# Kernel optimization log

Hardware: AMD Instinct MI355X
Metric: run time of the kernel (lower is better)

The kernel has to match this reference:

```python
import jax, jax.numpy as jnp
import numpy as np

N, C, HW, HEADS = 2048, 16, 8, 4
F = C * HW * HW  # 1024
E = 16384
EPS = 1e-5
NEG_SLOPE = 0.2


def _bn(x, g, b):
    # training-mode BatchNorm2d over (N, H, W)
    m = x.mean(axis=(0, 2, 3), keepdims=True)
    v = x.var(axis=(0, 2, 3), keepdims=True)
    return (x - m) * jax.lax.rsqrt(v + EPS) * g[None, :, None, None] + b[None, :, None, None]


def _conv1x1(x, w, b):
    # 1x1 conv == per-pixel linear: w is [out_c, in_c]
    return jnp.einsum('nchw,oc->nohw', x, w) + b[None, :, None, None]


def _gatv2(xf, edge_index, wl, bl, wr, br, att, bias_gat):
    # xf: [N, F] node features
    xl = (xf @ wl + bl).reshape(N, HEADS, F)  # source-side transform (lin_l)
    xr = (xf @ wr + br).reshape(N, HEADS, F)  # target-side transform (lin_r)
    src, dst = edge_index[0], edge_index[1]
    loops = jnp.arange(N)
    # PyG default: remove existing self loops (mask them) then add self loops
    src_f = jnp.concatenate([src, loops])
    dst_f = jnp.concatenate([dst, loops])
    valid = jnp.concatenate([src != dst, jnp.ones((N,), bool)])
    xj = xl[src_f]                                   # [E+N, HEADS, F] gather
    e = jax.nn.leaky_relu(xj + xr[dst_f], negative_slope=NEG_SLOPE)
    logits = jnp.einsum('ehf,hf->eh', e, att)        # [E+N, HEADS]
    logits = jnp.where(valid[:, None], logits, -jnp.inf)
    mx = jax.lax.stop_gradient(jax.ops.segment_max(logits, dst_f, num_segments=N))
    expv = jnp.where(valid[:, None], jnp.exp(logits - mx[dst_f]), 0.0)
    denom = jax.ops.segment_sum(expv, dst_f, num_segments=N)
    alpha = expv / denom[dst_f]                      # segment softmax over incoming edges
    out = jax.ops.segment_sum(alpha[:, :, None] * xj, dst_f, num_segments=N)  # [N, HEADS, F]
    return out.reshape(N, HEADS * F) + bias_gat


def setup_inputs() -> dict:
    key = jax.random.key(0)
    ks = jax.random.split(key, 8)
    s = 0.02
    return {
        'x': jax.random.normal(ks[0], (N, C, HW, HW), jnp.float32),
        'edge_index': jax.random.randint(ks[1], (2, E), 0, N),
        'w1': jax.random.normal(ks[2], (C, C), jnp.float32) * s,
        'b1': jnp.zeros((C,), jnp.float32),
        'g1': jnp.ones((C,), jnp.float32),
        'be1': jnp.zeros((C,), jnp.float32),
        'wl': jax.random.normal(ks[3], (F, HEADS * F), jnp.float32) * s,
        'bl': jnp.zeros((HEADS * F,), jnp.float32),
        'wr': jax.random.normal(ks[4], (F, HEADS * F), jnp.float32) * s,
        'br': jnp.zeros((HEADS * F,), jnp.float32),
        'att': jax.random.normal(ks[5], (HEADS, F), jnp.float32) * s,
        'bias_gat': jnp.zeros((HEADS * F,), jnp.float32),
        'w2': jax.random.normal(ks[6], (C, HEADS * C), jnp.float32) * s,
        'b2': jnp.zeros((C,), jnp.float32),
        'g2': jnp.ones((C,), jnp.float32),
        'be2': jnp.zeros((C,), jnp.float32),
    }


def reference(x, edge_index, w1, b1, g1, be1, wl, bl, wr, br, att, bias_gat, w2, b2, g2, be2):
    res = x
    y = _bn(_conv1x1(x, w1, b1), g1, be1)            # fc1: Conv2d 1x1 + BN
    yf = y.reshape(N, F)
    g = _gatv2(yf, edge_index, wl, bl, wr, br, att, bias_gat)
    g = g.reshape(N, HEADS * C, HW, HW)
    out = _bn(_conv1x1(g, w2, b2), g2, be2)          # fc2: Conv2d 1x1 + BN
    return out + res                                  # DropPath(0.0) == Identity
```

## Files before the change

### kernel.cpp

```cpp
#include <hip/hip_runtime.h>
#include <stdint.h>

#define N_NODES 2048
#define F_DIM   1024
#define HEADS   4
#define NF      4096
#define ROW     8192
#define E_EDGES 16384
#define MAXE    (E_EDGES + N_NODES)
#define BN_EPS  1e-5f
#define NSLOPE  0.2f

typedef unsigned short ushort_t;
typedef __attribute__((ext_vector_type(8))) short bf16x8;
typedef __attribute__((ext_vector_type(4))) float f32x4;
typedef __attribute__((ext_vector_type(8))) unsigned short us8;

__device__ __forceinline__ float b2f(unsigned short u) {
    union { unsigned int i; float f; } x; x.i = ((unsigned int)u) << 16; return x.f;
}
__device__ __forceinline__ unsigned short f2b(float f) {
    union { float f; unsigned int i; } x; x.f = f;
    unsigned int r = x.i + 0x7fffu + ((x.i >> 16) & 1u);
    return (unsigned short)(r >> 16);
}
__device__ __forceinline__ ushort_t ld_canon(const void* src, size_t i, int f32) {
    return f32 ? f2b(((const float*)src)[i]) : ((const ushort_t*)src)[i];
}
__device__ __forceinline__ float ld_f(const void* src, size_t i, int f32) {
    return f32 ? ((const float*)src)[i] : b2f(((const ushort_t*)src)[i]);
}

__device__ __forceinline__ int sniff_i64(const int* ei_raw, int* lds_flag) {
    int t = threadIdx.x;
    if (t < 64) {
        int nz = (ei_raw[2 * t + 1] != 0) ? 1 : 0;
        unsigned long long m = __ballot(nz);
        if (t == 0) *lds_flag = (m == 0ull) ? 1 : 0;
    }
    __syncthreads();
    return *lds_flag;
}

__global__ __launch_bounds__(256) void k_count(
    const int* __restrict__ ei_raw, const ushort_t* __restrict__ x_probe,
    int* __restrict__ counts, int* __restrict__ flags)
{
    __shared__ int sflag;
    int i64 = sniff_i64(ei_raw, &sflag);
    int t = threadIdx.x;
    if (blockIdx.x == 0 && t >= 64 && t < 96) {
        unsigned e = (x_probe[2 * (t - 64)] >> 7) & 0xFF;
        unsigned long long m = __ballot(e >= 0x90u);
        if (t == 64) flags[0] = (__popcll(m) >= 3) ? 1 : 0;
    }
    int idx = blockIdx.x * 256 + t;
    if (idx < E_EDGES) {
        int s = i64 ? ei_raw[2 * idx] : ei_raw[idx];
        int d = i64 ? ei_raw[2 * (E_EDGES + idx)] : ei_raw[E_EDGES + idx];
        if (s != d) atomicAdd(&counts[d], 1);
    } else if (idx < MAXE) {
        atomicAdd(&counts[idx - E_EDGES], 1);
    }
}

__global__ __launch_bounds__(256) void k_scan(
    const int* __restrict__ counts, int* __restrict__ offs, int* __restrict__ cursor)
{
    __shared__ int ts[256];
    int t = threadIdx.x;
    int loc[8]; int tot = 0;
    #pragma unroll
    for (int j = 0; j < 8; ++j) { loc[j] = counts[t * 8 + j]; tot += loc[j]; }
    ts[t] = tot; __syncthreads();
    for (int s = 1; s < 256; s <<= 1) {
        int v = (t >= s) ? ts[t - s] : 0;
        __syncthreads();
        ts[t] += v;
        __syncthreads();
    }
    int run = ts[t] - tot;
    #pragma unroll
    for (int j = 0; j < 8; ++j) {
        offs[t * 8 + j] = run; cursor[t * 8 + j] = run; run += loc[j];
    }
    if (t == 255) offs[2048] = run;
}

__global__ __launch_bounds__(256) void k_scatter(
    const int* __restrict__ ei_raw, int* __restrict__ cursor, int* __restrict__ esrc)
{
    __shared__ int sflag;
    int i64 = sniff_i64(ei_raw, &sflag);
    int idx = blockIdx.x * 256 + threadIdx.x;
    if (idx < E_EDGES) {
        int s = i64 ? ei_raw[2 * idx] : ei_raw[idx];
        int d = i64 ? ei_raw[2 * (E_EDGES + idx)] : ei_raw[E_EDGES + idx];
        if (s != d) esrc[atomicAdd(&cursor[d], 1)] = s;
    } else if (idx < MAXE) {
        int n = idx - E_EDGES;
        esrc[atomicAdd(&cursor[n], 1)] = n;
    }
}

__global__ __launch_bounds__(256) void k_fc1(
    const void* __restrict__ x, const void* __restrict__ w1, const void* __restrict__ b1,
    const int* __restrict__ flags,
    float* __restrict__ y0, float* __restrict__ ps, float* __restrict__ pq)
{
    __shared__ float xs[1024];
    __shared__ float sw[256];
    __shared__ float sb[16];
    int f32 = flags[0];
    int tid = threadIdx.x;
    sw[tid] = ld_f(w1, tid, f32);
    if (tid < 16) sb[tid] = ld_f(b1, tid, f32);
    int wave = tid >> 6, lane = tid & 63;
    float s[4] = {0,0,0,0}, q[4] = {0,0,0,0};
    for (int nn = 0; nn < 8; ++nn) {
        int n = blockIdx.x * 8 + nn;
        __syncthreads();
        #pragma unroll
        for (int i = 0; i < 4; ++i) {
            int idx = tid + i * 256;
            xs[idx] = ld_f(x, (size_t)n * 1024 + idx, f32);
        }
        __syncthreads();
        #pragma unroll
        for (int i = 0; i < 4; ++i) {
            int o = wave * 4 + i;
            float acc = sb[o];
            #pragma unroll
            for (int c = 0; c < 16; ++c) acc += xs[c * 64 + lane] * sw[o * 16 + c];
            y0[(size_t)n * 1024 + o * 64 + lane] = acc;
            s[i] += acc; q[i] += acc * acc;
        }
    }
    #pragma unroll
    for (int i = 0; i < 4; ++i)
        for (int mm = 1; mm < 64; mm <<= 1) {
            s[i] += __shfl_xor(s[i], mm);
            q[i] += __shfl_xor(q[i], mm);
        }
    if (lane == 0)
        #pragma unroll
        for (int i = 0; i < 4; ++i) {
            ps[blockIdx.x * 16 + wave * 4 + i] = s[i];
            pq[blockIdx.x * 16 + wave * 4 + i] = q[i];
        }
}

__global__ __launch_bounds__(256) void k_norm(
    const float* __restrict__ y0, const float* __restrict__ ps, const float* __restrict__ pq,
    const void* __restrict__ g1, const void* __restrict__ be1, const int* __restrict__ flags,
    ushort_t* __restrict__ xf)
{
    __shared__ float red[2][64];
    __shared__ float scs[16], shs[16];
    int f32 = flags[0];
    int t = threadIdx.x, lane = t & 63, wv = t >> 6;
    float s = 0.f, q = 0.f;
    #pragma unroll
    for (int i = 0; i < 16; ++i) { s += ps[i * 256 + t]; q += pq[i * 256 + t]; }
    s += __shfl_xor(s, 16); q += __shfl_xor(q, 16);
    s += __shfl_xor(s, 32); q += __shfl_xor(q, 32);
    if (lane < 16) { red[0][wv * 16 + lane] = s; red[1][wv * 16 + lane] = q; }
    __syncthreads();
    if (t < 16) {
        float S = red[0][t] + red[0][16 + t] + red[0][32 + t] + red[0][48 + t];
        float Q = red[1][t] + red[1][16 + t] + red[1][32 + t] + red[1][48 + t];
        const float inv = 1.0f / 131072.0f;
        float mean = S * inv;
        float var  = Q * inv - mean * mean;
        float sc = ld_f(g1, t, f32) * rsqrtf(var + BN_EPS);
        scs[t] = sc;
        shs[t] = ld_f(be1, t, f32) - mean * sc;
    }
    __syncthreads();
    int base = blockIdx.x * 4096;
    #pragma unroll
    for (int i = 0; i < 16; ++i) {
        int k = base + t + i * 256;
        int ch = (k >> 6) & 15;
        xf[k] = f2b(y0[k] * scs[ch] + shs[ch]);
    }
}

__global__ __launch_bounds__(256) void k_convT(
    const void* __restrict__ wl, const void* __restrict__ wr,
    const int* __restrict__ flags, ushort_t* __restrict__ wT)
{
    __shared__ ushort_t tl[64][65];
    int f32 = flags[0];
    const void* in = blockIdx.z ? wr : wl;
    ushort_t* outT = wT + (size_t)blockIdx.z * 4194304ull;
    int bx = blockIdx.x * 64, by = blockIdx.y * 64;
    #pragma unroll
    for (int i = 0; i < 16; ++i) {
        int idx = threadIdx.x + i * 256;
        int r = idx >> 6, c = idx & 63;
        tl[r][c] = ld_canon(in, (size_t)(by + r) * 4096 + bx + c, f32);
    }
    __syncthreads();
    #pragma unroll
    for (int i = 0; i < 16; ++i) {
        int idx = threadIdx.x + i * 256;
        int r = idx >> 6, c = idx & 63;
        outT[(size_t)(bx + r) * 1024 + by + c] = tl[c][r];
    }
}

__global__ __launch_bounds__(256) void k_gemm(
    const ushort_t* __restrict__ A, const ushort_t* __restrict__ BT,
    const void* __restrict__ blr, const void* __restrict__ brr,
    const int* __restrict__ flags, ushort_t* __restrict__ out)
{
    __shared__ __align__(16) ushort_t smem[16384];
    ushort_t* As0 = smem;
    ushort_t* As1 = smem + 4096;
    ushort_t* Bs0 = smem + 8192;
    ushort_t* Bs1 = smem + 12288;
    ushort_t* cs  = smem;
    int f32 = flags[0];
    int tid = threadIdx.x;
    int wv = tid >> 6, ln = tid & 63;
    int m0 = blockIdx.y * 128, n0 = blockIdx.x * 128;
    int wm = (wv >> 1) * 64, wn = (wv & 1) * 64;
    int lr = ln & 15, quad = ln >> 4;

    f32x4 acc[4][4];
    #pragma unroll
    for (int i = 0; i < 4; ++i)
        #pragma unroll
        for (int j = 0; j < 4; ++j) acc[i][j] = (f32x4){0.f, 0.f, 0.f, 0.f};

    for (int k0 = 0; k0 < 1024; k0 += 64) {
        #pragma unroll
        for (int i = 0; i < 2; ++i) {
            int cbase = i * 256 + wv * 64;
            int ci = cbase + ln;
            int m = ci >> 2, kc = ci & 3;
            const ushort_t* ga = A + (size_t)(m0 + m) * 1024 + k0 + kc * 8;
            __builtin_amdgcn_global_load_lds(
                (const __attribute__((address_space(1))) void*)ga,
                (__attribute__((address_space(3))) void*)(&As0[cbase * 8]), 16, 0, 0);
            __builtin_amdgcn_global_load_lds(
                (const __attribute__((address_space(1))) void*)(ga + 32),
                (__attribute__((address_space(3))) void*)(&As1[cbase * 8]), 16, 0, 0);
            const ushort_t* gb = BT + (size_t)(n0 + m) * 1024 + k0 + kc * 8;
            __builtin_amdgcn_global_load_lds(
                (const __attribute__((address_space(1))) void*)gb,
                (__attribute__((address_space(3))) void*)(&Bs0[cbase * 8]), 16, 0, 0);
            __builtin_amdgcn_global_load_lds(
                (const __attribute__((address_space(1))) void*)(gb + 32),
                (__attribute__((address_space(3))) void*)(&Bs1[cbase * 8]), 16, 0, 0);
        }
        __syncthreads();
        #pragma unroll
        for (int p = 0; p < 2; ++p) {
            const ushort_t* Ap = p ? As1 : As0;
            const ushort_t* Bp = p ? Bs1 : Bs0;
            bf16x8 af[4], bfr[4];
            #pragma unroll
            for (int i = 0; i < 4; ++i)
                af[i] = *(const bf16x8*)(&Ap[(wm + i * 16 + lr) * 32 + quad * 8]);
            #pragma unroll
            for (int j = 0; j < 4; ++j)
                bfr[j] = *(const bf16x8*)(&Bp[(wn + j * 16 + lr) * 32 + quad * 8]);
            #pragma unroll
            for (int i = 0; i < 4; ++i)
                #pragma unroll
                for (int j = 0; j < 4; ++j)
                    acc[i][j] = __builtin_amdgcn_mfma_f32_16x16x32_bf16(af[i], bfr[j], acc[i][j], 0, 0, 0);
        }
        __syncthreads();
    }
    float bj[4];
    #pragma unroll
    for (int j = 0; j < 4; ++j) {
        int colg = n0 + wn + j * 16 + lr;
        bj[j] = (colg < 4096) ? ld_f(blr, colg, f32) : ld_f(brr, colg - 4096, f32);
    }
    #pragma unroll
    for (int ph = 0; ph < 2; ++ph) {
        if ((wv >> 1) == ph) {
            #pragma unroll
            for (int i = 0; i < 4; ++i)
                #pragma unroll
                for (int j = 0; j < 4; ++j) {
                    int col = wn + j * 16 + lr;
                    #pragma unroll
                    for (int r = 0; r < 4; ++r)
                        cs[(i * 16 + quad * 4 + r) * 136 + col] = f2b(acc[i][j][r] + bj[j]);
                }
        }
        __syncthreads();
        #pragma unroll
        for (int rr = 0; rr < 4; ++rr) {
            int slot = rr * 256 + tid;
            int row = slot >> 4, seg = slot & 15;
            us8 v = *(const us8*)&cs[row * 136 + seg * 8];
            *(us8*)(out + (size_t)(m0 + ph * 64 + row) * ROW + n0 + seg * 8) = v;
        }
        __syncthreads();
    }
}

__global__ __launch_bounds__(256) void k_gat(
    const ushort_t* __restrict__ xlr,
    const void* __restrict__ att, const void* __restrict__ bg,
    const int* __restrict__ flags,
    const int* __restrict__ offsets, const int* __restrict__ esrc,
    ushort_t* __restrict__ g)
{
    int pair = blockIdx.x * 4 + (threadIdx.x >> 6);
    int d = pair >> 2, h = pair & 3;
    int l = threadIdx.x & 63;
    int f32 = flags[0];
    int off = offsets[d], deg = offsets[d + 1] - off;
    size_t hF = (size_t)h * F_DIM + l * 16;

    float xrv[16], attv[16];
    {
        const ushort_t* xp = xlr + ((size_t)d * ROW + NF + hF);
        us8 x0 = *(const us8*)xp, x1 = *(const us8*)(xp + 8);
        #pragma unroll
        for (int j = 0; j < 8; ++j) {
            xrv[j] = b2f(x0[j]); xrv[8 + j] = b2f(x1[j]);
            attv[j]     = ld_f(att, hF + j, f32);
            attv[8 + j] = ld_f(att, hF + 8 + j, f32);
        }
    }
    float acc[16];
    #pragma unroll
    for (int j = 0; j < 16; ++j) acc[j] = 0.f;
    float s_run = 0.f;

    for (int c0 = 0; c0 < deg; c0 += 64) {
        int cnt = min(64, deg - c0);
        int eidx = esrc[off + c0 + (l < cnt ? l : 0)];
        int e = 0;
        for (; e + 3 < cnt; e += 4) {
            int i0 = __shfl(eidx, e),     i1 = __shfl(eidx, e + 1);
            int i2 = __shfl(eidx, e + 2), i3 = __shfl(eidx, e + 3);
            const ushort_t* p0 = xlr + ((size_t)i0 * ROW + hF);
            const ushort_t* p1 = xlr + ((size_t)i1 * ROW + hF);
            const ushort_t* p2 = xlr + ((size_t)i2 * ROW + hF);
            const ushort_t* p3 = xlr + ((size_t)i3 * ROW + hF);
            us8 v0[4], v1[4];
            v0[0] = *(const us8*)p0; v1[0] = *(const us8*)(p0 + 8);
            v0[1] = *(const us8*)p1; v1[1] = *(const us8*)(p1 + 8);
            v0[2] = *(const us8*)p2; v1[2] = *(const us8*)(p2 + 8);
            v0[3] = *(const us8*)p3; v1[3] = *(const us8*)(p3 + 8);
            float tt[4];
            #pragma unroll
            for (int k = 0; k < 4; ++k) {
                float t0 = 0.f;
                #pragma unroll
                for (int j = 0; j < 8; ++j) {
                    float u;
                    u = b2f(v0[k][j]) + xrv[j];     u = u > 0.f ? u : NSLOPE * u; t0 += u * attv[j];
                    u = b2f(v1[k][j]) + xrv[8 + j]; u = u > 0.f ? u : NSLOPE * u; t0 += u * attv[8 + j];
                }
                tt[k] = t0;
            }
            #pragma unroll
            for (int mm = 1; mm < 64; mm <<= 1) {
                tt[0] += __shfl_xor(tt[0], mm);
                tt[1] += __shfl_xor(tt[1], mm);
                tt[2] += __shfl_xor(tt[2], mm);
                tt[3] += __shfl_xor(tt[3], mm);
            }
            float w0 = __expf(tt[0]), w1 = __expf(tt[1]);
            float w2v = __expf(tt[2]), w3 = __expf(tt[3]);
            s_run += w0 + w1 + w2v + w3;
            #pragma unroll
            for (int j = 0; j < 8; ++j) {
                acc[j]     += w0 * b2f(v0[0][j]) + w1 * b2f(v0[1][j])
                            + w2v * b2f(v0[2][j]) + w3 * b2f(v0[3][j]);
                acc[8 + j] += w0 * b2f(v1[0][j]) + w1 * b2f(v1[1][j])
                            + w2v * b2f(v1[2][j]) + w3 * b2f(v1[3][j]);
            }
        }
        for (; e < cnt; ++e) {
            int i0 = __shfl(eidx, e);
            const ushort_t* p = xlr + ((size_t)i0 * ROW + hF);
            us8 a0 = *(const us8*)p, a1 = *(const us8*)(p + 8);
            float t0 = 0.f;
            #pragma unroll
            for (int j = 0; j < 8; ++j) {
                float u;
                u = b2f(a0[j]) + xrv[j];     u = u > 0.f ? u : NSLOPE * u; t0 += u * attv[j];
                u = b2f(a1[j]) + xrv[8 + j]; u = u > 0.f ? u : NSLOPE * u; t0 += u * attv[8 + j];
            }
            #pragma unroll
            for (int mm = 1; mm < 64; mm <<= 1) t0 += __shfl_xor(t0, mm);
            float w0 = __expf(t0);
            s_run += w0;
            #pragma unroll
            for (int j = 0; j < 8; ++j) {
                acc[j]     += w0 * b2f(a0[j]);
                acc[8 + j] += w0 * b2f(a1[j]);
            }
        }
    }
    float inv = 1.0f / s_run;
    ushort_t* gp = g + ((size_t)d * NF + hF);
    us8 outv0, outv1;
    #pragma unroll
    for (int j = 0; j < 8; ++j) {
        outv0[j] = f2b(acc[j] * inv + ld_f(bg, hF + j, f32));
        outv1[j] = f2b(acc[8 + j] * inv + ld_f(bg, hF + 8 + j, f32));
    }
    *(us8*)gp = outv0;
    *(us8*)(gp + 8) = outv1;
}

__global__ __launch_bounds__(256) void k_fc2(
    const ushort_t* __restrict__ g, const void* __restrict__ w2, const void* __restrict__ b2,
    const int* __restrict__ flags,
    float* __restrict__ z, float* __restrict__ ps, float* __restrict__ pq)
{
    __shared__ float gs[4096];
    __shared__ float sw[1024];
    __shared__ float sb[16];
    int f32 = flags[0];
    int tid = threadIdx.x;
    #pragma unroll
    for (int i = 0; i < 4; ++i) sw[tid + i * 256] = ld_f(w2, tid + i * 256, f32);
    if (tid < 16) sb[tid] = ld_f(b2, tid, f32);
    int wave = tid >> 6, lane = tid & 63;
    float s[4] = {0,0,0,0}, q[4] = {0,0,0,0};
    for (int nn = 0; nn < 8; ++nn) {
        int n = blockIdx.x * 8 + nn;
        __syncthreads();
        {
            const ushort_t* gp = g + (size_t)n * 4096 + tid * 16;
            us8 v0 = *(const us8*)gp, v1 = *(const us8*)(gp + 8);
            #pragma unroll
            for (int j = 0; j < 8; ++j) {
                gs[tid * 16 + j] = b2f(v0[j]);
                gs[tid * 16 + 8 + j] = b2f(v1[j]);
            }
        }
        __syncthreads();
        #pragma unroll
        for (int i = 0; i < 4; ++i) {
            int o = wave * 4 + i;
            float acc = sb[o];
            #pragma unroll
            for (int k = 0; k < 64; ++k) acc += gs[k * 64 + lane] * sw[o * 64 + k];
            z[(size_t)n * 1024 + o * 64 + lane] = acc;
            s[i] += acc; q[i] += acc * acc;
        }
    }
    #pragma unroll
    for (int i = 0; i < 4; ++i)
        for (int mm = 1; mm < 64; mm <<= 1) {
            s[i] += __shfl_xor(s[i], mm);
            q[i] += __shfl_xor(q[i], mm);
        }
    if (lane == 0)
        #pragma unroll
        for (int i = 0; i < 4; ++i) {
            ps[blockIdx.x * 16 + wave * 4 + i] = s[i];
            pq[blockIdx.x * 16 + wave * 4 + i] = q[i];
        }
}

__global__ __launch_bounds__(256) void k_out(
    const float* __restrict__ z, const void* __restrict__ x,
    const float* __restrict__ ps, const float* __restrict__ pq,
    const void* __restrict__ g2, const void* __restrict__ be2,
    const int* __restrict__ flags, void* __restrict__ out)
{
    __shared__ float red[2][64];
    __shared__ float scs[16], shs[16];
    int f32 = flags[0];
    int t = threadIdx.x, lane = t & 63, wv = t >> 6;
    float s = 0.f, q = 0.f;
    #pragma unroll
    for (int i = 0; i < 16; ++i) { s += ps[i * 256 + t]; q += pq[i * 256 + t]; }
    s += __shfl_xor(s, 16); q += __shfl_xor(q, 16);
    s += __shfl_xor(s, 32); q += __shfl_xor(q, 32);
    if (lane < 16) { red[0][wv * 16 + lane] = s; red[1][wv * 16 + lane] = q; }
    __syncthreads();
    if (t < 16) {
        float S = red[0][t] + red[0][16 + t] + red[0][32 + t] + red[0][48 + t];
        float Q = red[1][t] + red[1][16 + t] + red[1][32 + t] + red[1][48 + t];
        const float inv = 1.0f / 131072.0f;
        float mean = S * inv;
        float var  = Q * inv - mean * mean;
        float sc = ld_f(g2, t, f32) * rsqrtf(var + BN_EPS);
        scs[t] = sc;
        shs[t] = ld_f(be2, t, f32) - mean * sc;
    }
    __syncthreads();
    size_t base = (size_t)blockIdx.x * 8192;
    #pragma unroll
    for (int i = 0; i < 32; ++i) {
        size_t k = base + t + i * 256;
        int ch = ((int)k >> 6) & 15;
        float val = z[k] * scs[ch] + shs[ch] + ld_f(x, k, f32);
        if (f32) ((float*)out)[k] = val;
        else     ((ushort_t*)out)[k] = f2b(val);
    }
}

extern "C" void kernel_launch(void* const* d_in, const int* in_sizes, int n_in,
                              void* d_out, int out_size, void* d_ws, size_t ws_size,
                              hipStream_t stream)
{
    const void* x   = d_in[0];
    const void* ei  = d_in[1];
    const void* w1  = d_in[2];
    const void* b1  = d_in[3];
    const void* g1  = d_in[4];
    const void* be1 = d_in[5];
    const void* wl  = d_in[6];
    const void* bl  = d_in[7];
    const void* wr  = d_in[8];
    const void* br  = d_in[9];
    const void* att = d_in[10];
    const void* bg  = d_in[11];
    const void* w2  = d_in[12];
    const void* b2  = d_in[13];
    const void* g2  = d_in[14];
    const void* be2 = d_in[15];
    (void)in_sizes; (void)n_in; (void)out_size; (void)ws_size;

    char* wsb = (char*)d_ws;
    size_t o = 0;
    auto alloc = [&](size_t bytes) -> void* {
        void* p = wsb + o;
        o = (o + bytes + 255) & ~(size_t)255;
        return p;
    };
    int*      flags = (int*)alloc(256);
    float*    y0    = (float*)alloc(2097152ull * 4);
    float*    z     = y0;
    ushort_t* xf    = (ushort_t*)alloc(2097152ull * 2);
    ushort_t* wT    = (ushort_t*)alloc(8388608ull * 2);
    ushort_t* gbuf  = wT;
    ushort_t* xlr   = (ushort_t*)alloc(16777216ull * 2);
    float* p1s = (float*)alloc(256 * 16 * 4);
    float* p1q = (float*)alloc(256 * 16 * 4);
    float* p2s = (float*)alloc(256 * 16 * 4);
    float* p2q = (float*)alloc(256 * 16 * 4);
    int* counts = (int*)alloc(2048 * 4);
    int* offs   = (int*)alloc(2049 * 4);
    int* cursor = (int*)alloc(2048 * 4);
    int* esrc   = (int*)alloc(MAXE * 4);

    hipMemsetAsync(counts, 0, 2048 * 4, stream);
    k_count<<<72, 256, 0, stream>>>((const int*)ei, (const ushort_t*)x, counts, flags);
    k_scan<<<1, 256, 0, stream>>>(counts, offs, cursor);
    k_scatter<<<72, 256, 0, stream>>>((const int*)ei, cursor, esrc);
    k_fc1<<<256, 256, 0, stream>>>(x, w1, b1, flags, y0, p1s, p1q);
    k_norm<<<512, 256, 0, stream>>>(y0, p1s, p1q, g1, be1, flags, xf);
    k_convT<<<dim3(64, 16, 2), 256, 0, stream>>>(wl, wr, flags, wT);
    k_gemm<<<dim3(64, 16), 256, 0, stream>>>(xf, wT, bl, br, flags, xlr);
    k_gat<<<N_NODES, 256, 0, stream>>>(xlr, att, bg, flags, offs, esrc, gbuf);
    k_fc2<<<256, 256, 0, stream>>>(gbuf, w2, b2, flags, z, p2s, p2q);
    k_out<<<256, 256, 0, stream>>>(z, x, p2s, p2q, g2, be2, flags, d_out);
}
```

Before: 290.7 us.

## Fold BN1 into GEMM weights, merge scan into scatter, prefetch GAT gathers

Several changes at once. The scan is merged into the scatter kernel: every block recomputes the prefix sum of the counts in shared memory, which removes one launch. The BN1 scale is folded into the transposed GAT weights, and its shift goes into a per-column bias correction computed from column sums, so the standalone normalize pass over y0 goes away and fc1 writes bf16 directly. The GAT kernel now runs one 64-thread block per (node, head) and double-buffers its gathered rows to overlap loads with compute. The risks are extra rounding from folding the scale into bf16 weights and a 16-term bias correction recomputed in every GEMM block.

```diff
diff --git a/kernel.cpp b/kernel.cpp
--- a/kernel.cpp
+++ b/kernel.cpp
@@ -64,10 +64,14 @@
     }
 }
 
-__global__ __launch_bounds__(256) void k_scan(
-    const int* __restrict__ counts, int* __restrict__ offs, int* __restrict__ cursor)
-{
+__global__ __launch_bounds__(256) void k_scatter(
+    const int* __restrict__ ei_raw, const int* __restrict__ counts,
+    int* __restrict__ cursor, int* __restrict__ offs, int* __restrict__ esrc)
+{
+    __shared__ int sflag;
+    __shared__ int offl[2048];
     __shared__ int ts[256];
+    int i64 = sniff_i64(ei_raw, &sflag);
     int t = threadIdx.x;
     int loc[8]; int tot = 0;
     #pragma unroll
@@ -81,32 +85,28 @@
     }
     int run = ts[t] - tot;
     #pragma unroll
-    for (int j = 0; j < 8; ++j) {
-        offs[t * 8 + j] = run; cursor[t * 8 + j] = run; run += loc[j];
-    }
-    if (t == 255) offs[2048] = run;
-}
-
-__global__ __launch_bounds__(256) void k_scatter(
-    const int* __restrict__ ei_raw, int* __restrict__ cursor, int* __restrict__ esrc)
-{
-    __shared__ int sflag;
-    int i64 = sniff_i64(ei_raw, &sflag);
-    int idx = blockIdx.x * 256 + threadIdx.x;
+    for (int j = 0; j < 8; ++j) { offl[t * 8 + j] = run; run += loc[j]; }
+    __syncthreads();
+    if (blockIdx.x == 0) {
+        #pragma unroll
+        for (int j = 0; j < 8; ++j) offs[t * 8 + j] = offl[t * 8 + j];
+        if (t == 255) offs[2048] = run;
+    }
+    int idx = blockIdx.x * 256 + t;
     if (idx < E_EDGES) {
         int s = i64 ? ei_raw[2 * idx] : ei_raw[idx];
         int d = i64 ? ei_raw[2 * (E_EDGES + idx)] : ei_raw[E_EDGES + idx];
-        if (s != d) esrc[atomicAdd(&cursor[d], 1)] = s;
+        if (s != d) esrc[offl[d] + atomicAdd(&cursor[d], 1)] = s;
     } else if (idx < MAXE) {
         int n = idx - E_EDGES;
-        esrc[atomicAdd(&cursor[n], 1)] = n;
+        esrc[offl[n] + atomicAdd(&cursor[n], 1)] = n;
     }
 }
 
 __global__ __launch_bounds__(256) void k_fc1(
     const void* __restrict__ x, const void* __restrict__ w1, const void* __restrict__ b1,
     const int* __restrict__ flags,
-    float* __restrict__ y0, float* __restrict__ ps, float* __restrict__ pq)
+    ushort_t* __restrict__ y0b, float* __restrict__ ps, float* __restrict__ pq)
 {
     __shared__ float xs[1024];
     __shared__ float sw[256];
@@ -132,7 +132,7 @@
             float acc = sb[o];
             #pragma unroll
             for (int c = 0; c < 16; ++c) acc += xs[c * 64 + lane] * sw[o * 16 + c];
-            y0[(size_t)n * 1024 + o * 64 + lane] = acc;
+            y0b[(size_t)n * 1024 + o * 64 + lane] = f2b(acc);
             s[i] += acc; q[i] += acc * acc;
         }
     }
@@ -150,51 +150,48 @@
         }
 }
 
-__global__ __launch_bounds__(256) void k_norm(
-    const float* __restrict__ y0, const float* __restrict__ ps, const float* __restrict__ pq,
-    const void* __restrict__ g1, const void* __restrict__ be1, const int* __restrict__ flags,
-    ushort_t* __restrict__ xf)
-{
-    __shared__ float red[2][64];
-    __shared__ float scs[16], shs[16];
-    int f32 = flags[0];
-    int t = threadIdx.x, lane = t & 63, wv = t >> 6;
+__global__ __launch_bounds__(256) void k_bnf1(
+    const float* __restrict__ ps, const float* __restrict__ pq,
+    const void* __restrict__ g1, const void* __restrict__ be1,
+    const int* __restrict__ flags, float* __restrict__ ss)
+{
+    __shared__ float rs[16][16], rq[16][16];
+    int f32 = flags[0];
+    int t = threadIdx.x;
+    int ch = t & 15, seg = t >> 4;
     float s = 0.f, q = 0.f;
-    #pragma unroll
-    for (int i = 0; i < 16; ++i) { s += ps[i * 256 + t]; q += pq[i * 256 + t]; }
-    s += __shfl_xor(s, 16); q += __shfl_xor(q, 16);
-    s += __shfl_xor(s, 32); q += __shfl_xor(q, 32);
-    if (lane < 16) { red[0][wv * 16 + lane] = s; red[1][wv * 16 + lane] = q; }
+    for (int j = 0; j < 16; ++j) {
+        int b = seg * 16 + j;
+        s += ps[b * 16 + ch]; q += pq[b * 16 + ch];
+    }
+    rs[seg][ch] = s; rq[seg][ch] = q;
     __syncthreads();
     if (t < 16) {
-        float S = red[0][t] + red[0][16 + t] + red[0][32 + t] + red[0][48 + t];
-        float Q = red[1][t] + red[1][16 + t] + red[1][32 + t] + red[1][48 + t];
+        float S = 0.f, Q = 0.f;
+        #pragma unroll
+        for (int g = 0; g < 16; ++g) { S += rs[g][t]; Q += rq[g][t]; }
         const float inv = 1.0f / 131072.0f;
         float mean = S * inv;
         float var  = Q * inv - mean * mean;
         float sc = ld_f(g1, t, f32) * rsqrtf(var + BN_EPS);
-        scs[t] = sc;
-        shs[t] = ld_f(be1, t, f32) - mean * sc;
-    }
-    __syncthreads();
-    int base = blockIdx.x * 4096;
-    #pragma unroll
-    for (int i = 0; i < 16; ++i) {
-        int k = base + t + i * 256;
-        int ch = (k >> 6) & 15;
-        xf[k] = f2b(y0[k] * scs[ch] + shs[ch]);
+        ss[t] = sc;
+        ss[16 + t] = ld_f(be1, t, f32) - mean * sc;
     }
 }
 
 __global__ __launch_bounds__(256) void k_convT(
     const void* __restrict__ wl, const void* __restrict__ wr,
-    const int* __restrict__ flags, ushort_t* __restrict__ wT)
+    const int* __restrict__ flags, const float* __restrict__ ss,
+    ushort_t* __restrict__ wT, float* __restrict__ csum)
 {
     __shared__ ushort_t tl[64][65];
+    __shared__ float red[4][64];
     int f32 = flags[0];
     const void* in = blockIdx.z ? wr : wl;
     ushort_t* outT = wT + (size_t)blockIdx.z * 4194304ull;
     int bx = blockIdx.x * 64, by = blockIdx.y * 64;
+    int ch = by >> 6;
+    float sc = ss[ch];
     #pragma unroll
     for (int i = 0; i < 16; ++i) {
         int idx = threadIdx.x + i * 256;
@@ -206,13 +203,23 @@
     for (int i = 0; i < 16; ++i) {
         int idx = threadIdx.x + i * 256;
         int r = idx >> 6, c = idx & 63;
-        outT[(size_t)(bx + r) * 1024 + by + c] = tl[c][r];
-    }
+        outT[(size_t)(bx + r) * 1024 + by + c] = f2b(b2f(tl[c][r]) * sc);
+    }
+    int c = threadIdx.x & 63, quarter = threadIdx.x >> 6;
+    float p = 0.f;
+    #pragma unroll
+    for (int rr = 0; rr < 16; ++rr) p += b2f(tl[quarter * 16 + rr][c]);
+    red[quarter][c] = p;
+    __syncthreads();
+    if (quarter == 0)
+        csum[(size_t)ch * 8192 + blockIdx.z * 4096 + bx + c]
+            = red[0][c] + red[1][c] + red[2][c] + red[3][c];
 }
 
 __global__ __launch_bounds__(256) void k_gemm(
     const ushort_t* __restrict__ A, const ushort_t* __restrict__ BT,
     const void* __restrict__ blr, const void* __restrict__ brr,
+    const float* __restrict__ ss, const float* __restrict__ csum,
     const int* __restrict__ flags, ushort_t* __restrict__ out)
 {
     __shared__ __align__(16) ushort_t smem[16384];
@@ -279,7 +286,12 @@
     #pragma unroll
     for (int j = 0; j < 4; ++j) {
         int colg = n0 + wn + j * 16 + lr;
-        bj[j] = (colg < 4096) ? ld_f(blr, colg, f32) : ld_f(brr, colg - 4096, f32);
+        float b0 = (colg < 4096) ? ld_f(blr, colg, f32) : ld_f(brr, colg - 4096, f32);
+        float corr = 0.f;
+        #pragma unroll
+        for (int ch = 0; ch < 16; ++ch)
+            corr += ss[16 + ch] * csum[(size_t)ch * 8192 + colg];
+        bj[j] = b0 + corr;
     }
     #pragma unroll
     for (int ph = 0; ph < 2; ++ph) {
@@ -306,16 +318,16 @@
     }
 }
 
-__global__ __launch_bounds__(256) void k_gat(
+__global__ __launch_bounds__(64) void k_gat(
     const ushort_t* __restrict__ xlr,
     const void* __restrict__ att, const void* __restrict__ bg,
     const int* __restrict__ flags,
     const int* __restrict__ offsets, const int* __restrict__ esrc,
     ushort_t* __restrict__ g)
 {
-    int pair = blockIdx.x * 4 + (threadIdx.x >> 6);
-    int d = pair >> 2, h = pair & 3;
-    int l = threadIdx.x & 63;
+    int bx = blockIdx.x;
+    int d = bx >> 2, h = bx & 3;
+    int l = threadIdx.x;
     int f32 = flags[0];
     int off = offsets[d], deg = offsets[d + 1] - off;
     size_t hF = (size_t)h * F_DIM + l * 16;
@@ -339,19 +351,22 @@
     for (int c0 = 0; c0 < deg; c0 += 64) {
         int cnt = min(64, deg - c0);
         int eidx = esrc[off + c0 + (l < cnt ? l : 0)];
-        int e = 0;
-        for (; e + 3 < cnt; e += 4) {
-            int i0 = __shfl(eidx, e),     i1 = __shfl(eidx, e + 1);
-            int i2 = __shfl(eidx, e + 2), i3 = __shfl(eidx, e + 3);
-            const ushort_t* p0 = xlr + ((size_t)i0 * ROW + hF);
-            const ushort_t* p1 = xlr + ((size_t)i1 * ROW + hF);
-            const ushort_t* p2 = xlr + ((size_t)i2 * ROW + hF);
-            const ushort_t* p3 = xlr + ((size_t)i3 * ROW + hF);
-            us8 v0[4], v1[4];
-            v0[0] = *(const us8*)p0; v1[0] = *(const us8*)(p0 + 8);
-            v0[1] = *(const us8*)p1; v1[1] = *(const us8*)(p1 + 8);
-            v0[2] = *(const us8*)p2; v1[2] = *(const us8*)(p2 + 8);
-            v0[3] = *(const us8*)p3; v1[3] = *(const us8*)(p3 + 8);
+        us8 A0[4], A1[4], B0[4], B1[4];
+        #pragma unroll
+        for (int k = 0; k < 4; ++k) {
+            int ii = min(k, cnt - 1);
+            const ushort_t* p = xlr + ((size_t)__shfl(eidx, ii) * ROW + hF);
+            A0[k] = *(const us8*)p; A1[k] = *(const us8*)(p + 8);
+        }
+        for (int e = 0; e < cnt; e += 4) {
+            if (e + 4 < cnt) {
+                #pragma unroll
+                for (int k = 0; k < 4; ++k) {
+                    int ii = min(e + 4 + k, cnt - 1);
+                    const ushort_t* p = xlr + ((size_t)__shfl(eidx, ii) * ROW + hF);
+                    B0[k] = *(const us8*)p; B1[k] = *(const us8*)(p + 8);
+                }
+            }
             float tt[4];
             #pragma unroll
             for (int k = 0; k < 4; ++k) {
@@ -359,8 +374,8 @@
                 #pragma unroll
                 for (int j = 0; j < 8; ++j) {
                     float u;
-                    u = b2f(v0[k][j]) + xrv[j];     u = u > 0.f ? u : NSLOPE * u; t0 += u * attv[j];
-                    u = b2f(v1[k][j]) + xrv[8 + j]; u = u > 0.f ? u : NSLOPE * u; t0 += u * attv[8 + j];
+                    u = b2f(A0[k][j]) + xrv[j];     u = u > 0.f ? u : NSLOPE * u; t0 += u * attv[j];
+                    u = b2f(A1[k][j]) + xrv[8 + j]; u = u > 0.f ? u : NSLOPE * u; t0 += u * attv[8 + j];
                 }
                 tt[k] = t0;
             }
@@ -371,36 +386,21 @@
                 tt[2] += __shfl_xor(tt[2], mm);
                 tt[3] += __shfl_xor(tt[3], mm);
             }
-            float w0 = __expf(tt[0]), w1 = __expf(tt[1]);
-            float w2v = __expf(tt[2]), w3 = __expf(tt[3]);
-            s_run += w0 + w1 + w2v + w3;
+            float w[4];
+            #pragma unroll
+            for (int k = 0; k < 4; ++k)
+                w[k] = (e + k < cnt) ? __expf(tt[k]) : 0.f;
+            s_run += w[0] + w[1] + w[2] + w[3];
             #pragma unroll
             for (int j = 0; j < 8; ++j) {
-                acc[j]     += w0 * b2f(v0[0][j]) + w1 * b2f(v0[1][j])
-                            + w2v * b2f(v0[2][j]) + w3 * b2f(v0[3][j]);
-                acc[8 + j] += w0 * b2f(v1[0][j]) + w1 * b2f(v1[1][j])
-                            + w2v * b2f(v1[2][j]) + w3 * b2f(v1[3][j]);
+                acc[j]     += w[0] * b2f(A0[0][j]) + w[1] * b2f(A0[1][j])
+                            + w[2] * b2f(A0[2][j]) + w[3] * b2f(A0[3][j]);
+                acc[8 + j] += w[0] * b2f(A1[0][j]) + w[1] * b2f(A1[1][j])
+                            + w[2] * b2f(A1[2][j]) + w[3] * b2f(A1[3][j]);
             }
-        }
-        for (; e < cnt; ++e) {
-            int i0 = __shfl(eidx, e);
-            const ushort_t* p = xlr + ((size_t)i0 * ROW + hF);
-            us8 a0 = *(const us8*)p, a1 = *(const us8*)(p + 8);
-            float t0 = 0.f;
-            #pragma unroll
-            for (int j = 0; j < 8; ++j) {
-                float u;
-                u = b2f(a0[j]) + xrv[j];     u = u > 0.f ? u : NSLOPE * u; t0 += u * attv[j];
-                u = b2f(a1[j]) + xrv[8 + j]; u = u > 0.f ? u : NSLOPE * u; t0 += u * attv[8 + j];
-            }
-            #pragma unroll
-            for (int mm = 1; mm < 64; mm <<= 1) t0 += __shfl_xor(t0, mm);
-            float w0 = __expf(t0);
-            s_run += w0;
-            #pragma unroll
-            for (int j = 0; j < 8; ++j) {
-                acc[j]     += w0 * b2f(a0[j]);
-                acc[8 + j] += w0 * b2f(a1[j]);
+            if (e + 4 < cnt) {
+                #pragma unroll
+                for (int k = 0; k < 4; ++k) { A0[k] = B0[k]; A1[k] = B1[k]; }
             }
         }
     }
@@ -537,9 +537,10 @@
         return p;
     };
     int*      flags = (int*)alloc(256);
-    float*    y0    = (float*)alloc(2097152ull * 4);
-    float*    z     = y0;
-    ushort_t* xf    = (ushort_t*)alloc(2097152ull * 2);
+    float*    ss    = (float*)alloc(32 * 4);
+    ushort_t* y0b   = (ushort_t*)alloc(2097152ull * 2);
+    float*    z     = (float*)alloc(2097152ull * 4);
+    float*    csum  = (float*)alloc(16 * 8192 * 4);
     ushort_t* wT    = (ushort_t*)alloc(8388608ull * 2);
     ushort_t* gbuf  = wT;
     ushort_t* xlr   = (ushort_t*)alloc(16777216ull * 2);
@@ -548,19 +549,18 @@
     float* p2s = (float*)alloc(256 * 16 * 4);
     float* p2q = (float*)alloc(256 * 16 * 4);
     int* counts = (int*)alloc(2048 * 4);
+    int* cursor = (int*)alloc(2048 * 4);
     int* offs   = (int*)alloc(2049 * 4);
-    int* cursor = (int*)alloc(2048 * 4);
     int* esrc   = (int*)alloc(MAXE * 4);
 
-    hipMemsetAsync(counts, 0, 2048 * 4, stream);
+    hipMemsetAsync(counts, 0, 2 * 2048 * 4, stream);
     k_count<<<72, 256, 0, stream>>>((const int*)ei, (const ushort_t*)x, counts, flags);
-    k_scan<<<1, 256, 0, stream>>>(counts, offs, cursor);
-    k_scatter<<<72, 256, 0, stream>>>((const int*)ei, cursor, esrc);
-    k_fc1<<<256, 256, 0, stream>>>(x, w1, b1, flags, y0, p1s, p1q);
-    k_norm<<<512, 256, 0, stream>>>(y0, p1s, p1q, g1, be1, flags, xf);
-    k_convT<<<dim3(64, 16, 2), 256, 0, stream>>>(wl, wr, flags, wT);
-    k_gemm<<<dim3(64, 16), 256, 0, stream>>>(xf, wT, bl, br, flags, xlr);
-    k_gat<<<N_NODES, 256, 0, stream>>>(xlr, att, bg, flags, offs, esrc, gbuf);
+    k_scatter<<<72, 256, 0, stream>>>((const int*)ei, counts, cursor, offs, esrc);
+    k_fc1<<<256, 256, 0, stream>>>(x, w1, b1, flags, y0b, p1s, p1q);
+    k_bnf1<<<1, 256, 0, stream>>>(p1s, p1q, g1, be1, flags, ss);
+    k_convT<<<dim3(64, 16, 2), 256, 0, stream>>>(wl, wr, flags, ss, wT, csum);
+    k_gemm<<<dim3(64, 16), 256, 0, stream>>>(y0b, wT, bl, br, ss, csum, flags, xlr);
+    k_gat<<<N_NODES * HEADS, 64, 0, stream>>>(xlr, att, bg, flags, offs, esrc, gbuf);
     k_fc2<<<256, 256, 0, stream>>>(gbuf, w2, b2, flags, z, p2s, p2q);
     k_out<<<256, 256, 0, stream>>>(z, x, p2s, p2q, g2, be2, flags, d_out);
 }
```

Result: faster. 284.9 us (-2.0%).
